# Kernel tuning notes

Measured on AMD Instinct MI355X. Metric: run time of the kernel, lower is better.

The kernel has to match this reference:

```python
import jax, jax.numpy as jnp
import numpy as np

B, C, D, H, W = 4, 256, 16, 16, 16


def setup_inputs() -> dict:
    key = jax.random.key(0)
    ks = jax.random.split(key, 9)
    s = 1.0 / np.sqrt(C)
    inp = {
        "x": jax.random.normal(ks[0], (B, C, D, H, W), dtype=jnp.float32),
        "wq": jax.random.normal(ks[1], (C, C), dtype=jnp.float32) * s,
        "bq": jax.random.normal(ks[2], (C,), dtype=jnp.float32) * 0.02,
        "wk": jax.random.normal(ks[3], (C, C), dtype=jnp.float32) * s,
        "bk": jax.random.normal(ks[4], (C,), dtype=jnp.float32) * 0.02,
        "wv": jax.random.normal(ks[5], (C, C), dtype=jnp.float32) * s,
        "bv": jax.random.normal(ks[6], (C,), dtype=jnp.float32) * 0.02,
        "wp": jax.random.normal(ks[7], (C, C), dtype=jnp.float32) * s,
        "bp": jax.random.normal(ks[8], (C,), dtype=jnp.float32) * 0.02,
    }
    return inp


def reference(x, wq, bq, wk, bk, wv, bv, wp, bp):
    b, c, d, h, w = x.shape
    xf = x.reshape(b, c, d * h * w)  # (B, C, N)
    # 1x1 Conv3d == per-voxel linear map over channels
    q = jnp.einsum('oc,bcn->bon', wq, xf) + bq[:, None]
    k = jnp.einsum('oc,bcn->bon', wk, xf) + bk[:, None]
    v = jnp.einsum('oc,bcn->bon', wv, xf) + bv[:, None]
    # scores[b,i,j] = q[:, :, i] . k[:, :, j], scaled AFTER the bmm (as in source)
    scores = jnp.einsum('bci,bcj->bij', q, k) * (c ** -0.5)
    p = jax.nn.softmax(scores, axis=2)  # (B, N, N), softmax over keys j
    # attention[b,c,i] = sum_j v[b,c,j] * p[b,i,j]
    attn = jnp.einsum('bcj,bij->bci', v, p)
    out = jnp.einsum('oc,bcn->bon', wp, attn) + bp[:, None]
    return x + out.reshape(b, c, d, h, w)
```

## Files before the change

### kernel.cpp

```cpp
#include <hip/hip_runtime.h>

typedef unsigned short u16;
typedef unsigned int u32;
typedef __bf16 v8bf __attribute__((ext_vector_type(8)));
typedef float v4f __attribute__((ext_vector_type(4)));

#define DEV __device__ __forceinline__

constexpr int CB = 4;
constexpr int C = 256;
constexpr int NN = 4096;
constexpr float LOG2E = 1.4426950408889634f;

DEV u16 f2bf(float f) {
  union { float f; u32 u; } v; v.f = f;
  u32 r = v.u + 0x7fffu + ((v.u >> 16) & 1u);
  return (u16)(r >> 16);
}
DEV float bf2f(u16 h) {
  union { u32 u; float f; } v; v.u = ((u32)h) << 16; return v.f;
}

DEV void dma16(const u16* g, const u16* lds_base) {
  __builtin_amdgcn_global_load_lds(
      (const __attribute__((address_space(1))) void*)(unsigned long long)g,
      (__attribute__((address_space(3))) void*)(u32)(unsigned long long)lds_base,
      16, 0, 0);
}

__global__ __launch_bounds__(256) void k_transpose(const float* __restrict__ x,
                                                   u16* __restrict__ xT) {
  __shared__ float tile[32][33];
  int b = blockIdx.z;
  int n0 = blockIdx.x * 32, c0 = blockIdx.y * 32;
  int tx = threadIdx.x & 31, ty = threadIdx.x >> 5;
  const float* xb = x + (long)b * C * NN;
#pragma unroll
  for (int r = 0; r < 4; ++r)
    tile[ty + r * 8][tx] = xb[(long)(c0 + ty + r * 8) * NN + n0 + tx];
  __syncthreads();
  u16* xTb = xT + (long)b * NN * C;
#pragma unroll
  for (int r = 0; r < 4; ++r)
    xTb[(long)(n0 + ty + r * 8) * C + c0 + tx] = f2bf(tile[tx][ty + r * 8]);
}

__global__ __launch_bounds__(256) void k_cvt4(const float* __restrict__ s0,
                                              const float* __restrict__ s1,
                                              const float* __restrict__ s2,
                                              const float* __restrict__ s3,
                                              u16* __restrict__ d0, u16* __restrict__ d1,
                                              u16* __restrict__ d2, u16* __restrict__ d3,
                                              float* __restrict__ Mbuf) {
  if (blockIdx.x == 0 && blockIdx.y == 0 && threadIdx.x < 8) Mbuf[threadIdx.x] = 0.f;
  int wsel = blockIdx.y;
  const float* s = wsel == 0 ? s0 : wsel == 1 ? s1 : wsel == 2 ? s2 : s3;
  u16* d = wsel == 0 ? d0 : wsel == 1 ? d1 : wsel == 2 ? d2 : d3;
  int i = blockIdx.x * 256 + threadIdx.x;
  d[i] = f2bf(s[i]);
}

DEV void stage_dma(const u16* __restrict__ g, const u16* lds, int w, int lane) {
#pragma unroll
  for (int i = 0; i < 8; ++i) {
    int idx = w * 8 + i;
    int r = idx * 2 + (lane >> 5);
    int cg = (lane & 31) ^ (r & 7);
    dma16(g + (long)r * 256 + cg * 8, lds + idx * 512);
  }
}

__global__ __launch_bounds__(256) void k_qkv(
    const u16* __restrict__ xT, const u16* __restrict__ wqb, const u16* __restrict__ wkb,
    const u16* __restrict__ wvb, const float* __restrict__ bq, const float* __restrict__ bk,
    const float* __restrict__ bv, u16* __restrict__ qO, u16* __restrict__ kO,
    u16* __restrict__ vO) {
  __shared__ __align__(16) u16 Ash[64 * 256];
  __shared__ __align__(16) u16 Bsh[64 * 256];
  int t = threadIdx.x, w = t >> 6, lane = t & 63, lr = lane & 15, q = lane >> 4;
  int m0 = blockIdx.x * 64, n0 = blockIdx.y * 64, b = blockIdx.z;
  const int xk = lr & 7;
  stage_dma(xT + (long)b * NN * C + (long)m0 * 256, Ash, w, lane);
  stage_dma(wqb + (long)n0 * 256, Bsh, w, lane);
  asm volatile("s_waitcnt vmcnt(0)\n\ts_barrier" ::: "memory");
#pragma unroll 1
  for (int wsel = 0; wsel < 3; ++wsel) {
    v4f acc[4];
#pragma unroll
    for (int nt = 0; nt < 4; ++nt)
#pragma unroll
      for (int r = 0; r < 4; ++r) acc[nt][r] = 0.f;
#pragma unroll
    for (int ks = 0; ks < 8; ++ks) {
      int cg = ((ks * 4 + q) ^ xk) << 3;
      v8bf a = *reinterpret_cast<const v8bf*>(Ash + (w * 16 + lr) * 256 + cg);
#pragma unroll
      for (int nt = 0; nt < 4; ++nt) {
        v8bf bb = *reinterpret_cast<const v8bf*>(Bsh + (nt * 16 + lr) * 256 + cg);
        acc[nt] = __builtin_amdgcn_mfma_f32_16x16x32_bf16(a, bb, acc[nt], 0, 0, 0);
      }
    }
    asm volatile("s_waitcnt lgkmcnt(0)\n\ts_barrier" ::: "memory");
    if (wsel < 2)
      stage_dma((wsel == 0 ? wkb : wvb) + (long)n0 * 256, Bsh, w, lane);
    const float* bias = wsel == 0 ? bq : wsel == 1 ? bk : bv;
#pragma unroll
    for (int nt = 0; nt < 4; ++nt) {
#pragma unroll
      for (int r = 0; r < 4; ++r) {
        int gm = m0 + w * 16 + q * 4 + r;
        int gn = n0 + nt * 16 + lr;
        float val = acc[nt][r] + bias[gn];
        if (wsel == 0) {
          qO[((long)b * NN + gm) * C + gn] = f2bf(val * (0.0625f * LOG2E));
        } else if (wsel == 1) {
          kO[((long)b * NN + gm) * C + gn] = f2bf(val);
        } else {
          vO[(long)b * C * NN + (long)gn * NN + gm] = f2bf(val);
        }
      }
    }
    asm volatile("s_waitcnt vmcnt(0)\n\ts_barrier" ::: "memory");
  }
}

__global__ __launch_bounds__(256) void k_maxnorm(const u16* __restrict__ qT,
                                                 const u16* __restrict__ kT,
                                                 float* __restrict__ Mbuf) {
  int b = blockIdx.z, tsel = blockIdx.y;
  const u16* src = (tsel ? kT : qT) + (long)b * NN * C;
  int row = blockIdx.x * 64 + (threadIdx.x >> 2);
  const uint4* pp =
      reinterpret_cast<const uint4*>(src + (long)row * C + (threadIdx.x & 3) * 64);
  float s = 0.f;
#pragma unroll
  for (int u = 0; u < 8; ++u) {
    uint4 d = pp[u];
    const u16* e = reinterpret_cast<const u16*>(&d);
#pragma unroll
    for (int i = 0; i < 8; ++i) { float f = bf2f(e[i]); s += f * f; }
  }
  s += __shfl_xor(s, 1, 64);
  s += __shfl_xor(s, 2, 64);
#pragma unroll
  for (int d2 = 4; d2 < 64; d2 <<= 1) s = fmaxf(s, __shfl_xor(s, d2, 64));
  if ((threadIdx.x & 63) == 0)
    atomicMax((u32*)(Mbuf + tsel * 4 + b), __float_as_uint(s));
}

__global__ __launch_bounds__(256) void k_gemm(
    const u16* __restrict__ A, long aStr, const u16* __restrict__ Bm, long bStr,
    const float* __restrict__ biasM, const float* __restrict__ biasN,
    const float* __restrict__ resid, long rStr, float scale,
    float* __restrict__ outF, u16* __restrict__ outH, long oStr, int ldm, int ldn) {
  __shared__ __align__(16) u16 Ash[64 * 256];
  __shared__ __align__(16) u16 Bsh[64 * 256];
  int t = threadIdx.x;
  int w = t >> 6, lane = t & 63, lr = lane & 15, q = lane >> 4;
  int m0 = blockIdx.x * 64, n0 = blockIdx.y * 64, b = blockIdx.z;
  const int xk = lr & 7;
  stage_dma(A + b * aStr + (long)m0 * 256, Ash, w, lane);
  stage_dma(Bm + b * bStr + (long)n0 * 256, Bsh, w, lane);
  asm volatile("s_waitcnt vmcnt(0)\n\ts_barrier" ::: "memory");
  v4f acc[4];
#pragma unroll
  for (int nt = 0; nt < 4; ++nt)
#pragma unroll
    for (int r = 0; r < 4; ++r) acc[nt][r] = 0.f;
#pragma unroll
  for (int ks = 0; ks < 8; ++ks) {
    int cg = ((ks * 4 + q) ^ xk) << 3;
    v8bf a = *reinterpret_cast<const v8bf*>(Ash + (w * 16 + lr) * 256 + cg);
#pragma unroll
    for (int nt = 0; nt < 4; ++nt) {
      v8bf bb = *reinterpret_cast<const v8bf*>(Bsh + (nt * 16 + lr) * 256 + cg);
      acc[nt] = __builtin_amdgcn_mfma_f32_16x16x32_bf16(a, bb, acc[nt], 0, 0, 0);
    }
  }
#pragma unroll
  for (int nt = 0; nt < 4; ++nt) {
#pragma unroll
    for (int r = 0; r < 4; ++r) {
      int gm = m0 + w * 16 + q * 4 + r;
      int gn = n0 + nt * 16 + lr;
      float val = acc[nt][r];
      if (biasM) val += biasM[gm];
      if (biasN) val += biasN[gn];
      val *= scale;
      long addr = b * oStr + (long)gm * ldm + (long)gn * ldn;
      if (resid) val += resid[b * rStr + (long)gm * ldm + (long)gn * ldn];
      if (outF) outF[addr] = val;
      else outH[addr] = f2bf(val);
    }
  }
}

DEV void flash_issue(const u16* kb, const u16* vb, const u16* kshb, const u16* vshb,
                     int j0, int w, int lane) {
#pragma unroll
  for (int i = 0; i < 4; ++i) {
    int idx = w * 4 + i;
    int kr = idx * 2 + (lane >> 5);
    int kc = (lane & 31) ^ (kr & 7);
    dma16(kb + (long)(j0 + kr) * 256 + kc * 8, kshb + idx * 512);
  }
#pragma unroll
  for (int i = 0; i < 4; ++i) {
    int idx = w * 4 + i;
    int vr = idx * 16 + (lane >> 2);
    int vc = (lane & 3) ^ ((vr ^ (vr >> 2)) & 3);
    dma16(vb + (long)vr * NN + j0 + vc * 8, vshb + idx * 512);
  }
}

__global__ __launch_bounds__(256, 2) void k_flash(const u16* __restrict__ qT,
                                                  const u16* __restrict__ kT,
                                                  const u16* __restrict__ V,
                                                  u16* __restrict__ op0,
                                                  u16* __restrict__ op1,
                                                  u16* __restrict__ op2,
                                                  u16* __restrict__ op3,
                                                  float* __restrict__ ml,
                                                  const float* __restrict__ Mbuf,
                                                  int span) {
  __shared__ __align__(16) u16 ksh[2][32 * 256];
  __shared__ __align__(16) u16 vsh[2][256 * 32];
  __shared__ __align__(16) u16 psh[4 * 16 * 40];
  int t = threadIdx.x;
  int w = t >> 6, lane = t & 63, lr = lane & 15, q = lane >> 4;
  int b = blockIdx.z, h = blockIdx.y;
  int i0 = blockIdx.x * 64;
  const u16* qb = qT + ((long)b * NN + i0 + w * 16) * C;
  const u16* kb = kT + (long)b * NN * C;
  const u16* vb = V + (long)b * C * NN;
  float M = sqrtf(Mbuf[b] * Mbuf[4 + b]) + 1.0f;

  v8bf qf[8];
#pragma unroll
  for (int ks = 0; ks < 8; ++ks)
    qf[ks] = *reinterpret_cast<const v8bf*>(qb + lr * C + ks * 32 + q * 8);

  v4f accO[16];
#pragma unroll
  for (int ct = 0; ct < 16; ++ct)
#pragma unroll
    for (int r = 0; r < 4; ++r) accO[ct][r] = 0.f;
  float lsum[4] = {0.f, 0.f, 0.f, 0.f};

  u16* pw = psh + w * 640;
  const int xk = lr & 7;
  const int xv = (lr ^ (lr >> 2)) & 3;

  int jstart = h * span;
  int niter = span >> 5;
  flash_issue(kb, vb, ksh[0], vsh[0], jstart, w, lane);
  int cur = 0;
#pragma unroll 1
  for (int it = 0; it < niter; ++it) {
    int j0 = jstart + (it << 5);
    int jn = (it + 1 < niter) ? j0 + 32 : jstart;
    asm volatile("s_waitcnt lgkmcnt(0)\n\ts_barrier" ::: "memory");
    flash_issue(kb, vb, ksh[cur ^ 1], vsh[cur ^ 1], jn, w, lane);
    asm volatile("s_waitcnt vmcnt(8)\n\ts_barrier" ::: "memory");

    const u16* kcur = ksh[cur];
    const u16* vcur = vsh[cur];
    v4f s[2];
#pragma unroll
    for (int jt = 0; jt < 2; ++jt)
#pragma unroll
      for (int r = 0; r < 4; ++r) s[jt][r] = 0.f;
#pragma unroll
    for (int ks = 0; ks < 8; ++ks) {
#pragma unroll
      for (int jt = 0; jt < 2; ++jt) {
        v8bf kf = *reinterpret_cast<const v8bf*>(
            kcur + (jt * 16 + lr) * 256 + (((ks * 4 + q) ^ xk) << 3));
        s[jt] = __builtin_amdgcn_mfma_f32_16x16x32_bf16(qf[ks], kf, s[jt], 0, 0, 0);
      }
    }

#pragma unroll
    for (int jt = 0; jt < 2; ++jt) {
#pragma unroll
      for (int r = 0; r < 4; ++r) {
        float p = exp2f(s[jt][r] - M);
        lsum[r] += p;
        u32 pb = (__float_as_uint(p) + 0x8000u) >> 16;
        pw[(q * 4 + r) * 40 + jt * 16 + lr] = (u16)pb;
      }
    }
    asm volatile("s_waitcnt lgkmcnt(0)" ::: "memory");
    v8bf pa = *reinterpret_cast<const v8bf*>(pw + lr * 40 + q * 8);
#pragma unroll
    for (int ct = 0; ct < 16; ++ct) {
      v8bf v0 = *reinterpret_cast<const v8bf*>(
          vcur + (ct * 16 + lr) * 32 + ((q ^ xv) << 3));
      accO[ct] = __builtin_amdgcn_mfma_f32_16x16x32_bf16(pa, v0, accO[ct], 0, 0, 0);
    }
    cur ^= 1;
  }

#pragma unroll
  for (int r = 0; r < 4; ++r) {
#pragma unroll
    for (int d = 1; d < 16; d <<= 1) lsum[r] += __shfl_xor(lsum[r], d, 64);
  }
  float inv[4];
#pragma unroll
  for (int r = 0; r < 4; ++r) inv[r] = 1.0f / lsum[r];
  u16* opp = h == 0 ? op0 : h == 1 ? op1 : h == 2 ? op2 : op3;
  u16* ob = opp + ((long)b * NN + i0 + w * 16) * C;
#pragma unroll
  for (int ct = 0; ct < 16; ++ct)
#pragma unroll
    for (int r = 0; r < 4; ++r)
      ob[(q * 4 + r) * C + ct * 16 + lr] = f2bf(accO[ct][r] * inv[r]);
  if (lr == 0) {
    long rbase = ((long)h * CB + b) * NN + i0 + w * 16 + q * 4;
#pragma unroll
    for (int r = 0; r < 4; ++r) {
      ml[(rbase + r) * 2] = M;
      ml[(rbase + r) * 2 + 1] = lsum[r];
    }
  }
}

__global__ __launch_bounds__(256) void k_combine(const u16* __restrict__ p0,
                                                 const u16* __restrict__ p1,
                                                 const u16* __restrict__ p2,
                                                 const u16* __restrict__ p3,
                                                 const float* __restrict__ ml,
                                                 u16* __restrict__ o, int js) {
  long row = (long)blockIdx.x * 8 + (threadIdx.x >> 5);
  int tc = (threadIdx.x & 31) * 8;
  float m[4], l[4];
  float mx = -3.0e38f;
  for (int h = 0; h < js; ++h) {
    m[h] = ml[((long)h * CB * NN + row) * 2];
    l[h] = ml[((long)h * CB * NN + row) * 2 + 1];
    mx = fmaxf(mx, m[h]);
  }
  float tot = 0.f, a[4];
  for (int h = 0; h < js; ++h) { a[h] = exp2f(m[h] - mx) * l[h]; tot += a[h]; }
  float inv = 1.f / tot;
  float acc[8];
#pragma unroll
  for (int i = 0; i < 8; ++i) acc[i] = 0.f;
  const u16* ps[4] = {p0, p1, p2, p3};
  for (int h = 0; h < js; ++h) {
    uint4 u = *reinterpret_cast<const uint4*>(ps[h] + row * C + tc);
    const u16* p = reinterpret_cast<const u16*>(&u);
    float wgt = a[h] * inv;
#pragma unroll
    for (int i = 0; i < 8; ++i) acc[i] += wgt * bf2f(p[i]);
  }
  u16 outv[8];
#pragma unroll
  for (int i = 0; i < 8; ++i) outv[i] = f2bf(acc[i]);
  *reinterpret_cast<uint4*>(o + row * C + tc) = *reinterpret_cast<const uint4*>(outv);
}

extern "C" void kernel_launch(void* const* d_in, const int* in_sizes, int n_in,
                              void* d_out, int out_size, void* d_ws, size_t ws_size,
                              hipStream_t stream) {
  const float* x = (const float*)d_in[0];
  const float* wq = (const float*)d_in[1];
  const float* bq = (const float*)d_in[2];
  const float* wk = (const float*)d_in[3];
  const float* bk = (const float*)d_in[4];
  const float* wv = (const float*)d_in[5];
  const float* bv = (const float*)d_in[6];
  const float* wp = (const float*)d_in[7];
  const float* bp = (const float*)d_in[8];
  float* out = (float*)d_out;
  char* ws = (char*)d_ws;

  const long SLOT = 8388608L;
  const size_t NEED4 = 524288UL + 7 * 8388608UL + 524288UL + 4096UL;
  int js = (ws_size >= NEED4) ? 4 : 2;

  u16* wqb = (u16*)(ws + 0);
  u16* wkb = (u16*)(ws + 131072L);
  u16* wvb = (u16*)(ws + 262144L);
  u16* wpb = (u16*)(ws + 393216L);
  char* base = ws + 524288L;
  u16* xT  = (u16*)(base);
  u16* qTw = (u16*)(base + 1 * SLOT);
  u16* kTw = (u16*)(base + 2 * SLOT);
  u16* vw  = (u16*)(base + 3 * SLOT);
  u16* op1 = (u16*)(base + 4 * SLOT);
  u16* op2 = js == 4 ? (u16*)(base + 5 * SLOT) : op1;
  u16* op3 = js == 4 ? (u16*)(base + 6 * SLOT) : op1;
  float* ml = (float*)(base + (js == 4 ? 7 : 5) * SLOT);
  float* Mbuf = ml + 131072;
  u16* op0 = xT;
  u16* oW  = qTw;

  k_cvt4<<<dim3(256, 4), 256, 0, stream>>>(wq, wk, wv, wp, wqb, wkb, wvb, wpb, Mbuf);
  k_transpose<<<dim3(128, 8, CB), 256, 0, stream>>>(x, xT);
  k_qkv<<<dim3(64, 4, CB), 256, 0, stream>>>(xT, wqb, wkb, wvb, bq, bk, bv, qTw, kTw, vw);
  k_maxnorm<<<dim3(64, 2, CB), 256, 0, stream>>>(qTw, kTw, Mbuf);
  k_flash<<<dim3(64, js, CB), 256, 0, stream>>>(qTw, kTw, vw, op0, op1, op2, op3, ml,
                                                Mbuf, NN / js);
  k_combine<<<2048, 256, 0, stream>>>(op0, op1, op2, op3, ml, oW, js);

  long nc = (long)NN * C;
  k_gemm<<<dim3(4, 64, CB), 256, 0, stream>>>(wpb, 0, oW, nc, bp, nullptr, x, nc,
                                              1.0f, out, nullptr, nc, NN, 1);
}
```

Measured before the change: 274.1 us.

## Split PV across warps by channel slice and coalesce V projection stores

In the flash kernel, each warp now computes a 64-channel slice of the output for all 64 query rows. It reads P for all four query sub-tiles from shared memory after a block barrier, so each V fragment is reused across four MFMAs instead of every warp reading all of V. Normalisation moves into the combine kernel, which now weights the unnormalised partials. The V projection epilogue stages its transposed tile through LDS so rows are written with 16-byte coalesced stores instead of scattered 2-byte ones. The cost is an extra barrier per iteration and larger P padding.

```diff
diff --git a/kernel.cpp b/kernel.cpp
--- a/kernel.cpp
+++ b/kernel.cpp
@@ -11,6 +11,7 @@
 constexpr int C = 256;
 constexpr int NN = 4096;
 constexpr float LOG2E = 1.4426950408889634f;
+constexpr int PST = 44;
 
 DEV u16 f2bf(float f) {
   union { float f; u32 u; } v; v.f = f;
@@ -101,26 +102,46 @@
       }
     }
     asm volatile("s_waitcnt lgkmcnt(0)\n\ts_barrier" ::: "memory");
-    if (wsel < 2)
+    if (wsel < 2) {
       stage_dma((wsel == 0 ? wkb : wvb) + (long)n0 * 256, Bsh, w, lane);
-    const float* bias = wsel == 0 ? bq : wsel == 1 ? bk : bv;
-#pragma unroll
-    for (int nt = 0; nt < 4; ++nt) {
-#pragma unroll
-      for (int r = 0; r < 4; ++r) {
-        int gm = m0 + w * 16 + q * 4 + r;
-        int gn = n0 + nt * 16 + lr;
-        float val = acc[nt][r] + bias[gn];
-        if (wsel == 0) {
-          qO[((long)b * NN + gm) * C + gn] = f2bf(val * (0.0625f * LOG2E));
-        } else if (wsel == 1) {
-          kO[((long)b * NN + gm) * C + gn] = f2bf(val);
-        } else {
-          vO[(long)b * C * NN + (long)gn * NN + gm] = f2bf(val);
+      const float* bias = wsel == 0 ? bq : bk;
+#pragma unroll
+      for (int nt = 0; nt < 4; ++nt) {
+#pragma unroll
+        for (int r = 0; r < 4; ++r) {
+          int gm = m0 + w * 16 + q * 4 + r;
+          int gn = n0 + nt * 16 + lr;
+          float val = acc[nt][r] + bias[gn];
+          if (wsel == 0) {
+            qO[((long)b * NN + gm) * C + gn] = f2bf(val * (0.0625f * LOG2E));
+          } else {
+            kO[((long)b * NN + gm) * C + gn] = f2bf(val);
+          }
         }
       }
-    }
-    asm volatile("s_waitcnt vmcnt(0)\n\ts_barrier" ::: "memory");
+      asm volatile("s_waitcnt vmcnt(0)\n\ts_barrier" ::: "memory");
+    } else {
+      u16* Vt = Ash;
+#pragma unroll
+      for (int nt = 0; nt < 4; ++nt) {
+#pragma unroll
+        for (int r = 0; r < 4; ++r) {
+          int gn_l = nt * 16 + lr;
+          int gm_l = w * 16 + q * 4 + r;
+          float val = acc[nt][r] + bv[n0 + gn_l];
+          Vt[gn_l * 72 + gm_l] = f2bf(val);
+        }
+      }
+      asm volatile("s_waitcnt lgkmcnt(0)\n\ts_barrier" ::: "memory");
+      int row = t >> 2;
+      u16* vrow = vO + (long)b * C * NN + (long)(n0 + row) * NN + m0;
+#pragma unroll
+      for (int s2 = 0; s2 < 2; ++s2) {
+        int seg = (t & 3) * 2 + s2;
+        *reinterpret_cast<uint4*>(vrow + seg * 8) =
+            *reinterpret_cast<const uint4*>(Vt + row * 72 + seg * 8);
+      }
+    }
   }
 }
 
@@ -225,7 +246,7 @@
                                                   int span) {
   __shared__ __align__(16) u16 ksh[2][32 * 256];
   __shared__ __align__(16) u16 vsh[2][256 * 32];
-  __shared__ __align__(16) u16 psh[4 * 16 * 40];
+  __shared__ __align__(16) u16 psh[64 * PST];
   int t = threadIdx.x;
   int w = t >> 6, lane = t & 63, lr = lane & 15, q = lane >> 4;
   int b = blockIdx.z, h = blockIdx.y;
@@ -247,7 +268,7 @@
     for (int r = 0; r < 4; ++r) accO[ct][r] = 0.f;
   float lsum[4] = {0.f, 0.f, 0.f, 0.f};
 
-  u16* pw = psh + w * 640;
+  u16* pw = psh + w * 16 * PST;
   const int xk = lr & 7;
   const int xv = (lr ^ (lr >> 2)) & 3;
 
@@ -287,16 +308,23 @@
         float p = exp2f(s[jt][r] - M);
         lsum[r] += p;
         u32 pb = (__float_as_uint(p) + 0x8000u) >> 16;
-        pw[(q * 4 + r) * 40 + jt * 16 + lr] = (u16)pb;
-      }
-    }
-    asm volatile("s_waitcnt lgkmcnt(0)" ::: "memory");
-    v8bf pa = *reinterpret_cast<const v8bf*>(pw + lr * 40 + q * 8);
-#pragma unroll
-    for (int ct = 0; ct < 16; ++ct) {
+        pw[(q * 4 + r) * PST + jt * 16 + lr] = (u16)pb;
+      }
+    }
+    asm volatile("s_waitcnt lgkmcnt(0)\n\ts_barrier" ::: "memory");
+    v8bf pa[4];
+#pragma unroll
+    for (int qs = 0; qs < 4; ++qs)
+      pa[qs] = *reinterpret_cast<const v8bf*>(psh + (qs * 16 + lr) * PST + q * 8);
+    const u16* vwp = vcur + w * 64 * 32;
+#pragma unroll
+    for (int cs = 0; cs < 4; ++cs) {
       v8bf v0 = *reinterpret_cast<const v8bf*>(
-          vcur + (ct * 16 + lr) * 32 + ((q ^ xv) << 3));
-      accO[ct] = __builtin_amdgcn_mfma_f32_16x16x32_bf16(pa, v0, accO[ct], 0, 0, 0);
+          vwp + (cs * 16 + lr) * 32 + ((q ^ xv) << 3));
+#pragma unroll
+      for (int qs = 0; qs < 4; ++qs)
+        accO[qs * 4 + cs] =
+            __builtin_amdgcn_mfma_f32_16x16x32_bf16(pa[qs], v0, accO[qs * 4 + cs], 0, 0, 0);
     }
     cur ^= 1;
   }
@@ -306,16 +334,16 @@
 #pragma unroll
     for (int d = 1; d < 16; d <<= 1) lsum[r] += __shfl_xor(lsum[r], d, 64);
   }
-  float inv[4];
-#pragma unroll
-  for (int r = 0; r < 4; ++r) inv[r] = 1.0f / lsum[r];
   u16* opp = h == 0 ? op0 : h == 1 ? op1 : h == 2 ? op2 : op3;
-  u16* ob = opp + ((long)b * NN + i0 + w * 16) * C;
-#pragma unroll
-  for (int ct = 0; ct < 16; ++ct)
-#pragma unroll
-    for (int r = 0; r < 4; ++r)
-      ob[(q * 4 + r) * C + ct * 16 + lr] = f2bf(accO[ct][r] * inv[r]);
+  u16* ob = opp + ((long)b * NN + i0) * C;
+#pragma unroll
+  for (int qs = 0; qs < 4; ++qs)
+#pragma unroll
+    for (int cs = 0; cs < 4; ++cs)
+#pragma unroll
+      for (int r = 0; r < 4; ++r)
+        ob[(qs * 16 + q * 4 + r) * C + w * 64 + cs * 16 + lr] =
+            f2bf(accO[qs * 4 + cs][r]);
   if (lr == 0) {
     long rbase = ((long)h * CB + b) * NN + i0 + w * 16 + q * 4;
 #pragma unroll
@@ -342,7 +370,7 @@
     mx = fmaxf(mx, m[h]);
   }
   float tot = 0.f, a[4];
-  for (int h = 0; h < js; ++h) { a[h] = exp2f(m[h] - mx) * l[h]; tot += a[h]; }
+  for (int h = 0; h < js; ++h) { a[h] = exp2f(m[h] - mx); tot += a[h] * l[h]; }
   float inv = 1.f / tot;
   float acc[8];
 #pragma unroll
```

After: 265.0 us. 3.3% less time.
